# Optimization experiments

Hardware: AMD Instinct MI355X
Metric: run time of the kernel (lower is better)

Reference implementation:

```python
import jax, jax.numpy as jnp
import numpy as np

RADIUS = 0.5
NSAMPLE = 32
RATIO = 0.25
HEADS = 8


def _ln(x, g, b, eps=1e-5):
    m = x.mean(-1, keepdims=True)
    v = ((x - m) ** 2).mean(-1, keepdims=True)
    return (x - m) / jnp.sqrt(v + eps) * g + b


def _fps(xyz, M):
    """Farthest point sampling (start at index 0, matches pytorch3d default). Non-differentiable."""
    xyz = jax.lax.stop_gradient(xyz)  # mirrors @torch.no_grad
    B, N, _ = xyz.shape

    def step(carry, _):
        mind, last = carry  # (B,N), (B,)
        lastp = jnp.take_along_axis(xyz, last[:, None, None], axis=1)  # (B,1,3)
        d = jnp.sum((xyz - lastp) ** 2, axis=-1)  # (B,N)
        mind = jnp.minimum(mind, d)
        nxt = jnp.argmax(mind, axis=1).astype(jnp.int32)
        return (mind, nxt), last

    init = (jnp.full((B, N), jnp.inf, xyz.dtype), jnp.zeros((B,), jnp.int32))
    _, idx = jax.lax.scan(step, init, None, length=M)
    return idx.T  # (B,M)


def setup_inputs() -> dict:
    key = jax.random.key(0)
    ks = jax.random.split(key, 12)
    B, N, Cin, C = 2, 8192, 64, 128
    w = lambda i, shape: jax.random.normal(ks[i], shape, jnp.float32) * 0.02
    return {
        "xyz": jax.random.normal(ks[0], (B, N, 3), jnp.float32),
        "feats": jax.random.normal(ks[1], (B, N, Cin), jnp.float32),
        "W_in": w(2, (Cin, C)), "b_in": jnp.zeros((C,), jnp.float32),
        "ln_in_g": jnp.ones((C,), jnp.float32), "ln_in_b": jnp.zeros((C,), jnp.float32),
        "W_pos": w(3, (3, C)), "b_pos": jnp.zeros((C,), jnp.float32),
        "Wq": w(4, (C, C)), "bq": jnp.zeros((C,), jnp.float32),
        "Wk": w(5, (C, C)), "bk": jnp.zeros((C,), jnp.float32),
        "Wv": w(6, (C, C)), "bv": jnp.zeros((C,), jnp.float32),
        "Wo": w(7, (C, C)), "bo": jnp.zeros((C,), jnp.float32),
        "ln1_g": jnp.ones((C,), jnp.float32), "ln1_b": jnp.zeros((C,), jnp.float32),
        "W1": w(8, (C, 4 * C)), "b1": jnp.zeros((4 * C,), jnp.float32),
        "W2": w(9, (4 * C, C)), "b2": jnp.zeros((C,), jnp.float32),
        "ln2_g": jnp.ones((C,), jnp.float32), "ln2_b": jnp.zeros((C,), jnp.float32),
        "out_g": jnp.ones((C,), jnp.float32), "out_b": jnp.zeros((C,), jnp.float32),
    }


def reference(xyz, feats, W_in, b_in, ln_in_g, ln_in_b, W_pos, b_pos,
              Wq, bq, Wk, bk, Wv, bv, Wo, bo, ln1_g, ln1_b,
              W1, b1, W2, b2, ln2_g, ln2_b, out_g, out_b):
    B, N, _ = xyz.shape
    M = max(1, int(round(N * RATIO)))
    K = NSAMPLE

    # --- FPS centroids ---
    ctr_idx = _fps(xyz, M)  # (B,M) int32
    ctr_xyz = xyz[jnp.arange(B)[:, None], ctr_idx]  # (B,M,3)

    # --- ball query: first K points (by index) within radius; -1 where missing ---
    d2 = jnp.sum((ctr_xyz[:, :, None, :] - xyz[:, None, :, :]) ** 2, axis=-1)  # (B,M,N)
    within = d2 < RADIUS * RADIUS
    cand = jnp.where(within, jnp.arange(N, dtype=jnp.int32)[None, None, :], N)
    first_k = jnp.sort(cand, axis=-1)[..., :K]  # (B,M,K)
    raw_idx = jnp.where(first_k < N, first_k, -1)
    neigh_idx = jnp.where(raw_idx < 0, ctr_idx[:, :, None], raw_idx)  # fill pads with centroid

    b3 = jnp.arange(B)[:, None, None]
    neigh_xyz = xyz[b3, neigh_idx]     # (B,M,K,3)
    neigh_feats = feats[b3, neigh_idx]  # (B,M,K,Cin)

    # --- in_proj: Linear -> LayerNorm -> ReLU ---
    h = jax.nn.relu(_ln(neigh_feats @ W_in + b_in, ln_in_g, ln_in_b))  # (B,M,K,C)
    C = h.shape[-1]
    BM = B * M
    pad = (raw_idx < 0).reshape(BM, K)  # key padding mask

    # --- local transformer layer (coords -> positional embedding, post-norm) ---
    x = h.reshape(BM, K, C) + (neigh_xyz.reshape(BM, K, 3) @ W_pos + b_pos)
    H = HEADS
    Dh = C // H
    split = lambda t: t.reshape(BM, K, H, Dh).transpose(0, 2, 1, 3)  # (BM,H,K,Dh)
    q, k, v = split(x @ Wq + bq), split(x @ Wk + bk), split(x @ Wv + bv)
    scores = jnp.einsum('bhqd,bhkd->bhqk', q, k) / np.sqrt(Dh)
    scores = jnp.where(pad[:, None, None, :], -1e9, scores)
    attn = jax.nn.softmax(scores, axis=-1)
    o = jnp.einsum('bhqk,bhkd->bhqd', attn, v).transpose(0, 2, 1, 3).reshape(BM, K, C)
    x = _ln(x + o @ Wo + bo, ln1_g, ln1_b)
    x = _ln(x + jax.nn.relu(x @ W1 + b1) @ W2 + b2, ln2_g, ln2_b)

    # --- max-pool over neighbourhood, out LayerNorm ---
    pooled = _ln(x.max(axis=1).reshape(B, M, C), out_g, out_b)
    return ctr_xyz, pooled
```

## Files before the change

### kernel.cpp

```cpp
#include <hip/hip_runtime.h>
#include <math.h>

#define N_PTS 8192
#define BATCH 2
#define M_CTR 2048
#define KNB   32
#define CIN   64
#define CH    128
#define NHEAD 8
#define DH    16

typedef __attribute__((ext_vector_type(4))) float f32x4;
typedef __attribute__((ext_vector_type(8))) short bf16x8;

template<int CTRL>
__device__ __forceinline__ unsigned long long dpp_max_u64(unsigned long long k) {
  int lo = (int)(unsigned)k;
  int hi = (int)(k >> 32);
  int lo2 = __builtin_amdgcn_update_dpp(0, lo, CTRL, 0xF, 0xF, true);
  int hi2 = __builtin_amdgcn_update_dpp(0, hi, CTRL, 0xF, 0xF, true);
  unsigned long long o = ((unsigned long long)(unsigned)hi2 << 32) | (unsigned)lo2;
  return o > k ? o : k;
}

__device__ __forceinline__ unsigned long long swz16_max_u64(unsigned long long k) {
  int lo = (int)(unsigned)k;
  int hi = (int)(k >> 32);
  int lo2 = __builtin_amdgcn_ds_swizzle(lo, 0x401F);
  int hi2 = __builtin_amdgcn_ds_swizzle(hi, 0x401F);
  unsigned long long o = ((unsigned long long)(unsigned)hi2 << 32) | (unsigned)lo2;
  return o > k ? o : k;
}

__device__ __forceinline__ unsigned long long maxu64(unsigned long long a,
                                                     unsigned long long b) {
  return a > b ? a : b;
}

__global__ __launch_bounds__(512, 1) void fps_kernel(const float* __restrict__ xyz,
                                                     int* __restrict__ ctrIdx,
                                                     float* __restrict__ outCtr) {
  __shared__ float4 sxyz[N_PTS];
  __shared__ int    cidx[M_CTR];
  __shared__ __align__(16) unsigned long long candK[2][8];

  const int b = blockIdx.x;
  const int t = threadIdx.x;
  const int lane = t & 63;
  const int w = t >> 6;
  const float* xb = xyz + (size_t)b * N_PTS * 3;

  float px[16], py[16], pz[16], mind[16];
#pragma unroll
  for (int s = 0; s < 16; ++s) {
    int pt = t + s * 512;
    float x = xb[pt * 3 + 0];
    float y = xb[pt * 3 + 1];
    float z = xb[pt * 3 + 2];
    px[s] = x; py[s] = y; pz[s] = z;
    mind[s] = INFINITY;
    sxyz[pt] = make_float4(x, y, z, 0.f);
  }
  unsigned lo16[16];
#pragma unroll
  for (int s = 0; s < 16; ++s) lo16[s] = ~(unsigned)(t + s * 512);
  __syncthreads();

  int last = 0;
  for (int m = 0; m < M_CTR; ++m) {
    if (t == 0) cidx[m] = last;
    float4 lp = sxyz[last];
#pragma unroll
    for (int s = 0; s < 16; ++s) {
      float dx = __fsub_rn(px[s], lp.x);
      float dy = __fsub_rn(py[s], lp.y);
      float dz = __fsub_rn(pz[s], lp.z);
      float d2 = __fadd_rn(__fadd_rn(__fmul_rn(dx, dx), __fmul_rn(dy, dy)),
                           __fmul_rn(dz, dz));
      mind[s] = fminf(mind[s], d2);
    }
    unsigned long long key[16];
#pragma unroll
    for (int s = 0; s < 16; ++s)
      key[s] = ((unsigned long long)__float_as_uint(mind[s]) << 32) | lo16[s];
#pragma unroll
    for (int i = 0; i < 8; ++i) key[i] = maxu64(key[i], key[i + 8]);
#pragma unroll
    for (int i = 0; i < 4; ++i) key[i] = maxu64(key[i], key[i + 4]);
    key[0] = maxu64(key[0], key[2]);
    key[1] = maxu64(key[1], key[3]);
    unsigned long long k0 = maxu64(key[0], key[1]);
    k0 = dpp_max_u64<0xB1>(k0);
    k0 = dpp_max_u64<0x4E>(k0);
    k0 = dpp_max_u64<0x141>(k0);
    k0 = dpp_max_u64<0x140>(k0);
    k0 = swz16_max_u64(k0);
    k0 = maxu64(k0, (unsigned long long)__shfl_xor((unsigned long long)k0, 32, 64));
    const int buf = m & 1;
    if (lane == 0) candK[buf][w] = k0;
    __syncthreads();
    const ulonglong2* ck = (const ulonglong2*)&candK[buf][0];
    ulonglong2 c0v = ck[0], c1v = ck[1], c2v = ck[2], c3v = ck[3];
    unsigned long long m0 = maxu64(c0v.x, c0v.y);
    unsigned long long m1 = maxu64(c1v.x, c1v.y);
    unsigned long long m2 = maxu64(c2v.x, c2v.y);
    unsigned long long m3 = maxu64(c3v.x, c3v.y);
    unsigned long long best = maxu64(maxu64(m0, m1), maxu64(m2, m3));
    last = (int)(~(unsigned)best);
  }
  __syncthreads();
  for (int m = t; m < M_CTR; m += 512) {
    int ci = cidx[m];
    ctrIdx[b * M_CTR + m] = ci;
    float4 c = sxyz[ci];
    float* o = outCtr + (size_t)(b * M_CTR + m) * 3;
    o[0] = c.x; o[1] = c.y; o[2] = c.z;
  }
}

__global__ __launch_bounds__(256) void ballq_kernel(const float* __restrict__ xyz,
                                                    const int* __restrict__ ctrIdx,
                                                    int* __restrict__ rawIdx) {
  const int cm   = blockIdx.x * 4 + (threadIdx.x >> 6);
  const int lane = threadIdx.x & 63;
  const int b    = cm >> 11;
  const float* xb = xyz + (size_t)b * N_PTS * 3;
  const int ci = ctrIdx[cm];
  const float cx = xb[ci * 3 + 0], cy = xb[ci * 3 + 1], cz = xb[ci * 3 + 2];
  int* out = rawIdx + (size_t)cm * KNB;
  int have = 0;
  for (int base = 0; base < N_PTS; base += 64) {
    int pt = base + lane;
    float dx = __fsub_rn(cx, xb[pt * 3 + 0]);
    float dy = __fsub_rn(cy, xb[pt * 3 + 1]);
    float dz = __fsub_rn(cz, xb[pt * 3 + 2]);
    float d2 = __fadd_rn(__fadd_rn(__fmul_rn(dx, dx), __fmul_rn(dy, dy)),
                         __fmul_rn(dz, dz));
    bool hit = d2 < 0.25f;
    unsigned long long mask = __ballot(hit);
    if (hit) {
      int rank = have + __popcll(mask & ((1ull << lane) - 1ull));
      if (rank < KNB) out[rank] = pt;
    }
    have += __popcll(mask);
    if (have >= KNB) break;
  }
  if (lane < KNB && lane >= have) out[lane] = -1;
}

__device__ __forceinline__ unsigned short f2bf(float f) {
  unsigned u = __float_as_uint(f);
  unsigned r = (u + 0x7FFFu + ((u >> 16) & 1u)) >> 16;
  return (unsigned short)r;
}
__device__ __forceinline__ float bf2f(unsigned short s) {
  return __uint_as_float(((unsigned)s) << 16);
}

__global__ __launch_bounds__(256) void prep_kernel(const float* __restrict__ W_in,
    const float* __restrict__ Wq, const float* __restrict__ Wk,
    const float* __restrict__ Wv, const float* __restrict__ Wo,
    const float* __restrict__ W1, const float* __restrict__ W2,
    short* __restrict__ wsW) {
  int i = blockIdx.x * 256 + threadIdx.x;
  if (i >= 204800) return;
  const float* src; int K, C, off;
  if (i < 8192)        { src = W_in; K = 64;  C = 128; off = i; }
  else if (i < 24576)  { src = Wq;   K = 128; C = 128; off = i - 8192; }
  else if (i < 40960)  { src = Wk;   K = 128; C = 128; off = i - 24576; }
  else if (i < 57344)  { src = Wv;   K = 128; C = 128; off = i - 40960; }
  else if (i < 73728)  { src = Wo;   K = 128; C = 128; off = i - 57344; }
  else if (i < 139264) { src = W1;   K = 128; C = 512; off = i - 73728; }
  else                 { src = W2;   K = 512; C = 128; off = i - 139264; }
  int c = off / K, k = off - c * K;
  wsW[i] = (short)f2bf(src[(size_t)k * C + c]);
}

#define XS  136
#define VTS 40
#define PS  264

struct SAParams {
  const float* xyz; const float* feats;
  const float* b_in; const float* ln_in_g; const float* ln_in_b;
  const float* W_pos; const float* b_pos;
  const float* bq; const float* bk; const float* bv; const float* bo;
  const float* ln1_g; const float* ln1_b;
  const float* b1; const float* b2;
  const float* ln2_g; const float* ln2_b; const float* out_g; const float* out_b;
  const short* wsW;
  const int* ctrIdx; const int* rawIdx;
  float* out;
};

template<int C>
__device__ __forceinline__ float dppf(float v) {
  return __int_as_float(__builtin_amdgcn_update_dpp(0, __float_as_int(v), C, 0xF, 0xF, true));
}
__device__ __forceinline__ float red16_add(float v) {
  v += dppf<0xB1>(v);  v += dppf<0x4E>(v);
  v += dppf<0x141>(v); v += dppf<0x140>(v);
  return v;
}
__device__ __forceinline__ float red16_max(float v) {
  v = fmaxf(v, dppf<0xB1>(v));  v = fmaxf(v, dppf<0x4E>(v));
  v = fmaxf(v, dppf<0x141>(v)); v = fmaxf(v, dppf<0x140>(v));
  return v;
}

template<int NCT, int NKS>
__device__ __forceinline__ void mm_mfma(const short* __restrict__ albase, int lstr,
                                        const short* __restrict__ wt, int wK,
                                        f32x4 (&acc)[NCT], int l15, int lg) {
#pragma unroll
  for (int ks = 0; ks < NKS; ++ks) {
    bf16x8 a = *(const bf16x8*)(albase + l15 * lstr + ks * 32 + lg * 8);
#pragma unroll
    for (int ct = 0; ct < NCT; ++ct) {
      bf16x8 bf = *(const bf16x8*)(wt + (size_t)(ct * 16 + l15) * wK + ks * 32 + lg * 8);
      acc[ct] = __builtin_amdgcn_mfma_f32_16x16x32_bf16(a, bf, acc[ct], 0, 0, 0);
    }
  }
}

__global__ __launch_bounds__(128, 1) void sa_kernel(SAParams p) {
  __shared__ short sm[3 * 32 * XS + 128 * VTS + 32 * PS];
  __shared__ float nxs[32], nys[32], nzs[32];
  __shared__ int   nidx[32];
  __shared__ unsigned padmaskS;
  __shared__ float psum[2][2];

  short* const xb  = sm;
  short* const qb  = sm + 32 * XS;
  short* const kb  = sm + 2 * 32 * XS;
  short* const vT  = sm + 3 * 32 * XS;
  short* const Pb  = sm + 3 * 32 * XS + 128 * VTS;
  short* const fsb = Pb;
  short* const ob  = qb;
  short* const hb  = kb;

  const int t    = threadIdx.x;
  const int lane = t & 63;
  const int rt   = t >> 6;
  const int l15  = lane & 15;
  const int lg   = lane >> 4;
  const int cm   = blockIdx.x;
  const int b    = cm >> 11;
  const short* arow = 0;

  if (t < 32) {
    int raw = p.rawIdx[(size_t)cm * KNB + t];
    int ci  = p.ctrIdx[cm];
    int ni  = (raw < 0) ? ci : raw;
    nidx[t] = ni;
    const float* q = p.xyz + ((size_t)b * N_PTS + ni) * 3;
    nxs[t] = q[0]; nys[t] = q[1]; nzs[t] = q[2];
  }
  if (t < 64) {
    bool isPad = (t < 32) ? (p.rawIdx[(size_t)cm * KNB + t] < 0) : false;
    unsigned long long m = __ballot(isPad);
    if (t == 0) padmaskS = (unsigned)m;
  }
  __syncthreads();

  {
    int row = t >> 2;
    int cs  = (t & 3) * 16;
    const float* src = p.feats + ((size_t)b * N_PTS + nidx[row]) * CIN + cs;
    float4 f0 = *(const float4*)(src + 0);
    float4 f1 = *(const float4*)(src + 4);
    float4 f2 = *(const float4*)(src + 8);
    float4 f3 = *(const float4*)(src + 12);
    unsigned short u[16];
#pragma unroll
    for (int j = 0; j < 4; ++j) {
      u[j]      = f2bf((&f0.x)[j]); u[4 + j]  = f2bf((&f1.x)[j]);
      u[8 + j]  = f2bf((&f2.x)[j]); u[12 + j] = f2bf((&f3.x)[j]);
    }
    uint4 w0, w1;
    unsigned* uw = (unsigned*)&w0;
#pragma unroll
    for (int j = 0; j < 8; ++j) ((unsigned*)&w0)[j < 4 ? j : j] = 0;
    (void)uw;
    unsigned packed[8];
#pragma unroll
    for (int j = 0; j < 8; ++j) packed[j] = (unsigned)u[2 * j] | ((unsigned)u[2 * j + 1] << 16);
    w0 = make_uint4(packed[0], packed[1], packed[2], packed[3]);
    w1 = make_uint4(packed[4], packed[5], packed[6], packed[7]);
    *(uint4*)(fsb + row * 72 + cs)     = w0;
    *(uint4*)(fsb + row * 72 + cs + 8) = w1;
  }
  __syncthreads();

  const unsigned padmask = padmaskS;
  float rowxyz[3][4];
#pragma unroll
  for (int r = 0; r < 4; ++r) {
    int row = rt * 16 + lg * 4 + r;
    rowxyz[0][r] = nxs[row]; rowxyz[1][r] = nys[row]; rowxyz[2][r] = nzs[row];
  }

  {
    f32x4 acc[8] = {};
    mm_mfma<8, 2>(fsb + rt * 16 * 72, 72, p.wsW + 0, 64, acc, l15, lg);
    float s[4] = {}, sq[4] = {};
#pragma unroll
    for (int ct = 0; ct < 8; ++ct) {
      float bia = p.b_in[ct * 16 + l15];
#pragma unroll
      for (int r = 0; r < 4; ++r) {
        acc[ct][r] += bia;
        s[r] += acc[ct][r]; sq[r] += acc[ct][r] * acc[ct][r];
      }
    }
    float mean[4], inv[4];
#pragma unroll
    for (int r = 0; r < 4; ++r) {
      float S = red16_add(s[r]), SQ = red16_add(sq[r]);
      mean[r] = S * (1.0f / CH);
      float var = fmaxf(SQ * (1.0f / CH) - mean[r] * mean[r], 0.f);
      inv[r] = rsqrtf(var + 1e-5f);
    }
#pragma unroll
    for (int ct = 0; ct < 8; ++ct) {
      int c = ct * 16 + l15;
      float g  = p.ln_in_g[c], bt = p.ln_in_b[c];
      float w0 = p.W_pos[0 * CH + c], w1 = p.W_pos[1 * CH + c];
      float w2 = p.W_pos[2 * CH + c], bp = p.b_pos[c];
#pragma unroll
      for (int r = 0; r < 4; ++r) {
        int row = rt * 16 + lg * 4 + r;
        float h = (acc[ct][r] - mean[r]) * inv[r] * g + bt;
        h = fmaxf(h, 0.f);
        float pos = fmaf(rowxyz[0][r], w0, fmaf(rowxyz[1][r], w1,
                    fmaf(rowxyz[2][r], w2, bp)));
        xb[row * XS + c] = (short)f2bf(h + pos);
      }
    }
  }
  __syncthreads();

  arow = xb + rt * 16 * XS;
  {
    f32x4 acc[8] = {};
    mm_mfma<8, 4>(arow, XS, p.wsW + 8192, 128, acc, l15, lg);
#pragma unroll
    for (int ct = 0; ct < 8; ++ct) {
      int c = ct * 16 + l15;
      float bia = p.bq[c];
#pragma unroll
      for (int r = 0; r < 4; ++r)
        qb[(rt * 16 + lg * 4 + r) * XS + c] = (short)f2bf((acc[ct][r] + bia) * 0.25f);
    }
  }
  {
    f32x4 acc[8] = {};
    mm_mfma<8, 4>(arow, XS, p.wsW + 24576, 128, acc, l15, lg);
#pragma unroll
    for (int ct = 0; ct < 8; ++ct) {
      int c = ct * 16 + l15;
      float bia = p.bk[c];
#pragma unroll
      for (int r = 0; r < 4; ++r)
        kb[(rt * 16 + lg * 4 + r) * XS + c] = (short)f2bf(acc[ct][r] + bia);
    }
  }
  {
    f32x4 acc[8] = {};
    mm_mfma<8, 4>(arow, XS, p.wsW + 40960, 128, acc, l15, lg);
#pragma unroll
    for (int ct = 0; ct < 8; ++ct) {
      int c = ct * 16 + l15;
      float bia = p.bv[c];
#pragma unroll
      for (int r = 0; r < 4; ++r)
        vT[c * VTS + rt * 16 + lg * 4 + r] = (short)f2bf(acc[ct][r] + bia);
    }
  }
  __syncthreads();

  {
    bool pad0 = (padmask >> l15) & 1u;
    bool pad1 = (padmask >> (16 + l15)) & 1u;
    const bf16x8 z = {0, 0, 0, 0, 0, 0, 0, 0};
#pragma unroll
    for (int h = 0; h < NHEAD; ++h) {
      bf16x8 a = *(const bf16x8*)(qb + (rt * 16 + l15) * XS + h * DH + (lg & 1) * 8);
      if (lg >= 2) a = z;
      bf16x8 b0 = *(const bf16x8*)(kb + (l15) * XS + h * DH + (lg & 1) * 8);
      bf16x8 b1 = *(const bf16x8*)(kb + (16 + l15) * XS + h * DH + (lg & 1) * 8);
      f32x4 s0 = {}, s1 = {};
      s0 = __builtin_amdgcn_mfma_f32_16x16x32_bf16(a, b0, s0, 0, 0, 0);
      s1 = __builtin_amdgcn_mfma_f32_16x16x32_bf16(a, b1, s1, 0, 0, 0);
#pragma unroll
      for (int r = 0; r < 4; ++r) {
        float v0 = pad0 ? -1e9f : s0[r];
        float v1 = pad1 ? -1e9f : s1[r];
        float mx = red16_max(fmaxf(v0, v1));
        float e0 = __expf(v0 - mx), e1 = __expf(v1 - mx);
        float sum = red16_add(e0 + e1);
        float isum = 1.0f / sum;
        int row = rt * 16 + lg * 4 + r;
        Pb[row * PS + h * 32 + l15]      = (short)f2bf(e0 * isum);
        Pb[row * PS + h * 32 + 16 + l15] = (short)f2bf(e1 * isum);
      }
    }
  }
  __syncthreads();

  {
#pragma unroll
    for (int h = 0; h < NHEAD; ++h) {
      bf16x8 a  = *(const bf16x8*)(Pb + (rt * 16 + l15) * PS + h * 32 + lg * 8);
      bf16x8 bf = *(const bf16x8*)(vT + (h * DH + l15) * VTS + lg * 8);
      f32x4 o = {};
      o = __builtin_amdgcn_mfma_f32_16x16x32_bf16(a, bf, o, 0, 0, 0);
#pragma unroll
      for (int r = 0; r < 4; ++r)
        ob[(rt * 16 + lg * 4 + r) * XS + h * DH + l15] = (short)f2bf(o[r]);
    }
  }

  {
    f32x4 acc[8] = {};
    mm_mfma<8, 4>(ob + rt * 16 * XS, XS, p.wsW + 57344, 128, acc, l15, lg);
    float s[4] = {}, sq[4] = {};
#pragma unroll
    for (int ct = 0; ct < 8; ++ct) {
      int c = ct * 16 + l15;
      float bia = p.bo[c];
#pragma unroll
      for (int r = 0; r < 4; ++r) {
        int row = rt * 16 + lg * 4 + r;
        acc[ct][r] += bia + bf2f((unsigned short)xb[row * XS + c]);
        s[r] += acc[ct][r]; sq[r] += acc[ct][r] * acc[ct][r];
      }
    }
    float mean[4], inv[4];
#pragma unroll
    for (int r = 0; r < 4; ++r) {
      float S = red16_add(s[r]), SQ = red16_add(sq[r]);
      mean[r] = S * (1.0f / CH);
      float var = fmaxf(SQ * (1.0f / CH) - mean[r] * mean[r], 0.f);
      inv[r] = rsqrtf(var + 1e-5f);
    }
#pragma unroll
    for (int ct = 0; ct < 8; ++ct) {
      int c = ct * 16 + l15;
      float g = p.ln1_g[c], bt = p.ln1_b[c];
#pragma unroll
      for (int r = 0; r < 4; ++r) {
        int row = rt * 16 + lg * 4 + r;
        xb[row * XS + c] = (short)f2bf((acc[ct][r] - mean[r]) * inv[r] * g + bt);
      }
    }
  }

  {
    f32x4 acc2[8] = {};
#pragma unroll
    for (int cb = 0; cb < 4; ++cb) {
      f32x4 acch[8] = {};
      mm_mfma<8, 4>(xb + rt * 16 * XS, XS, p.wsW + 73728 + cb * 128 * 128, 128,
                    acch, l15, lg);
#pragma unroll
      for (int ct = 0; ct < 8; ++ct) {
        int c = ct * 16 + l15;
        float bia = p.b1[cb * 128 + c];
#pragma unroll
        for (int r = 0; r < 4; ++r)
          hb[(rt * 16 + lg * 4 + r) * XS + c] = (short)f2bf(fmaxf(acch[ct][r] + bia, 0.f));
      }
      __syncthreads();
      mm_mfma<8, 4>(hb + rt * 16 * XS, XS, p.wsW + 139264 + cb * 128, 512,
                    acc2, l15, lg);
      __syncthreads();
    }
    float s[4] = {}, sq[4] = {};
#pragma unroll
    for (int ct = 0; ct < 8; ++ct) {
      int c = ct * 16 + l15;
      float bia = p.b2[c];
#pragma unroll
      for (int r = 0; r < 4; ++r) {
        int row = rt * 16 + lg * 4 + r;
        acc2[ct][r] += bia + bf2f((unsigned short)xb[row * XS + c]);
        s[r] += acc2[ct][r]; sq[r] += acc2[ct][r] * acc2[ct][r];
      }
    }
    float mean[4], inv[4];
#pragma unroll
    for (int r = 0; r < 4; ++r) {
      float S = red16_add(s[r]), SQ = red16_add(sq[r]);
      mean[r] = S * (1.0f / CH);
      float var = fmaxf(SQ * (1.0f / CH) - mean[r] * mean[r], 0.f);
      inv[r] = rsqrtf(var + 1e-5f);
    }
#pragma unroll
    for (int ct = 0; ct < 8; ++ct) {
      int c = ct * 16 + l15;
      float g = p.ln2_g[c], bt = p.ln2_b[c];
#pragma unroll
      for (int r = 0; r < 4; ++r) {
        int row = rt * 16 + lg * 4 + r;
        xb[row * XS + c] = (short)f2bf((acc2[ct][r] - mean[r]) * inv[r] * g + bt);
      }
    }
  }
  __syncthreads();

  {
    float mx = -INFINITY;
#pragma unroll 8
    for (int r = 0; r < KNB; ++r) mx = fmaxf(mx, bf2f((unsigned short)xb[r * XS + t]));
    float s = mx, sq = mx * mx;
#pragma unroll
    for (int off = 1; off < 64; off <<= 1) {
      s  += __shfl_xor(s,  off, 64);
      sq += __shfl_xor(sq, off, 64);
    }
    if (lane == 0) { psum[rt][0] = s; psum[rt][1] = sq; }
    __syncthreads();
    float S = psum[0][0] + psum[1][0];
    float SQ = psum[0][1] + psum[1][1];
    float mean = S * (1.0f / CH);
    float var = fmaxf(SQ * (1.0f / CH) - mean * mean, 0.f);
    float inv = rsqrtf(var + 1e-5f);
    p.out[(size_t)BATCH * M_CTR * 3 + (size_t)cm * CH + t] =
        (mx - mean) * inv * p.out_g[t] + p.out_b[t];
  }
}

extern "C" void kernel_launch(void* const* d_in, const int* in_sizes, int n_in,
                              void* d_out, int out_size, void* d_ws, size_t ws_size,
                              hipStream_t stream) {
  const float* xyz     = (const float*)d_in[0];
  const float* feats   = (const float*)d_in[1];
  const float* W_in    = (const float*)d_in[2];
  const float* b_in    = (const float*)d_in[3];
  const float* ln_in_g = (const float*)d_in[4];
  const float* ln_in_b = (const float*)d_in[5];
  const float* W_pos   = (const float*)d_in[6];
  const float* b_pos   = (const float*)d_in[7];
  const float* Wq      = (const float*)d_in[8];
  const float* bq      = (const float*)d_in[9];
  const float* Wk      = (const float*)d_in[10];
  const float* bk      = (const float*)d_in[11];
  const float* Wv      = (const float*)d_in[12];
  const float* bv      = (const float*)d_in[13];
  const float* Wo      = (const float*)d_in[14];
  const float* bo      = (const float*)d_in[15];
  const float* ln1_g   = (const float*)d_in[16];
  const float* ln1_b   = (const float*)d_in[17];
  const float* W1      = (const float*)d_in[18];
  const float* b1      = (const float*)d_in[19];
  const float* W2      = (const float*)d_in[20];
  const float* b2      = (const float*)d_in[21];
  const float* ln2_g   = (const float*)d_in[22];
  const float* ln2_b   = (const float*)d_in[23];
  const float* out_g   = (const float*)d_in[24];
  const float* out_b   = (const float*)d_in[25];
  float* out = (float*)d_out;

  int* wsCtr = (int*)d_ws;
  int* wsRaw = wsCtr + BATCH * M_CTR;
  short* wsW = (short*)(wsRaw + BATCH * M_CTR * KNB);

  prep_kernel<<<(204800 + 255) / 256, 256, 0, stream>>>(W_in, Wq, Wk, Wv, Wo,
                                                        W1, W2, wsW);
  fps_kernel<<<BATCH, 512, 0, stream>>>(xyz, wsCtr, out);
  ballq_kernel<<<(BATCH * M_CTR) / 4, 256, 0, stream>>>(xyz, wsCtr, wsRaw);

  SAParams p{xyz, feats, b_in, ln_in_g, ln_in_b, W_pos, b_pos,
             bq, bk, bv, bo, ln1_g, ln1_b, b1, b2,
             ln2_g, ln2_b, out_g, out_b,
             wsW, wsCtr, wsRaw, out};
  sa_kernel<<<BATCH * M_CTR, 128, 0, stream>>>(p);
}
```

Measured before the change: 2.348 ms.

## Widen FPS to 1024 threads with LDS atomicMax reduction and inline center writes

```diff
diff --git a/kernel.cpp b/kernel.cpp
--- a/kernel.cpp
+++ b/kernel.cpp
@@ -37,84 +37,67 @@
   return a > b ? a : b;
 }
 
-__global__ __launch_bounds__(512, 1) void fps_kernel(const float* __restrict__ xyz,
-                                                     int* __restrict__ ctrIdx,
-                                                     float* __restrict__ outCtr) {
+__global__ __launch_bounds__(1024, 1) void fps_kernel(const float* __restrict__ xyz,
+                                                      int* __restrict__ ctrIdx,
+                                                      float* __restrict__ outCtr) {
   __shared__ float4 sxyz[N_PTS];
-  __shared__ int    cidx[M_CTR];
-  __shared__ __align__(16) unsigned long long candK[2][8];
+  __shared__ unsigned long long redK[4];
 
   const int b = blockIdx.x;
   const int t = threadIdx.x;
   const int lane = t & 63;
-  const int w = t >> 6;
   const float* xb = xyz + (size_t)b * N_PTS * 3;
 
-  float px[16], py[16], pz[16], mind[16];
-#pragma unroll
-  for (int s = 0; s < 16; ++s) {
-    int pt = t + s * 512;
+  float px[8], py[8], pz[8], mind[8];
+  unsigned lo8[8];
+#pragma unroll
+  for (int s = 0; s < 8; ++s) {
+    int pt = t + s * 1024;
     float x = xb[pt * 3 + 0];
     float y = xb[pt * 3 + 1];
     float z = xb[pt * 3 + 2];
     px[s] = x; py[s] = y; pz[s] = z;
     mind[s] = INFINITY;
+    lo8[s] = ~(unsigned)pt;
     sxyz[pt] = make_float4(x, y, z, 0.f);
   }
-  unsigned lo16[16];
-#pragma unroll
-  for (int s = 0; s < 16; ++s) lo16[s] = ~(unsigned)(t + s * 512);
+  if (t < 3) redK[t] = 0ull;
   __syncthreads();
 
   int last = 0;
   for (int m = 0; m < M_CTR; ++m) {
-    if (t == 0) cidx[m] = last;
     float4 lp = sxyz[last];
-#pragma unroll
-    for (int s = 0; s < 16; ++s) {
+    if (t == 0) {
+      ctrIdx[b * M_CTR + m] = last;
+      float* o = outCtr + (size_t)(b * M_CTR + m) * 3;
+      o[0] = lp.x; o[1] = lp.y; o[2] = lp.z;
+    }
+    unsigned long long c0 = 0ull, c1 = 0ull;
+#pragma unroll
+    for (int s = 0; s < 8; ++s) {
       float dx = __fsub_rn(px[s], lp.x);
       float dy = __fsub_rn(py[s], lp.y);
       float dz = __fsub_rn(pz[s], lp.z);
       float d2 = __fadd_rn(__fadd_rn(__fmul_rn(dx, dx), __fmul_rn(dy, dy)),
                            __fmul_rn(dz, dz));
-      mind[s] = fminf(mind[s], d2);
-    }
-    unsigned long long key[16];
-#pragma unroll
-    for (int s = 0; s < 16; ++s)
-      key[s] = ((unsigned long long)__float_as_uint(mind[s]) << 32) | lo16[s];
-#pragma unroll
-    for (int i = 0; i < 8; ++i) key[i] = maxu64(key[i], key[i + 8]);
-#pragma unroll
-    for (int i = 0; i < 4; ++i) key[i] = maxu64(key[i], key[i + 4]);
-    key[0] = maxu64(key[0], key[2]);
-    key[1] = maxu64(key[1], key[3]);
-    unsigned long long k0 = maxu64(key[0], key[1]);
+      float mn = fminf(mind[s], d2);
+      mind[s] = mn;
+      unsigned long long key =
+          ((unsigned long long)__float_as_uint(mn) << 32) | lo8[s];
+      if (s & 1) c1 = maxu64(c1, key); else c0 = maxu64(c0, key);
+    }
+    unsigned long long k0 = maxu64(c0, c1);
     k0 = dpp_max_u64<0xB1>(k0);
     k0 = dpp_max_u64<0x4E>(k0);
     k0 = dpp_max_u64<0x141>(k0);
     k0 = dpp_max_u64<0x140>(k0);
     k0 = swz16_max_u64(k0);
-    k0 = maxu64(k0, (unsigned long long)__shfl_xor((unsigned long long)k0, 32, 64));
-    const int buf = m & 1;
-    if (lane == 0) candK[buf][w] = k0;
+    const int buf = m % 3;
+    if ((lane & 31) == 0)
+      atomicMax((unsigned long long*)&redK[buf], k0);
+    if (t == 1) redK[(m + 1) % 3] = 0ull;
     __syncthreads();
-    const ulonglong2* ck = (const ulonglong2*)&candK[buf][0];
-    ulonglong2 c0v = ck[0], c1v = ck[1], c2v = ck[2], c3v = ck[3];
-    unsigned long long m0 = maxu64(c0v.x, c0v.y);
-    unsigned long long m1 = maxu64(c1v.x, c1v.y);
-    unsigned long long m2 = maxu64(c2v.x, c2v.y);
-    unsigned long long m3 = maxu64(c3v.x, c3v.y);
-    unsigned long long best = maxu64(maxu64(m0, m1), maxu64(m2, m3));
-    last = (int)(~(unsigned)best);
-  }
-  __syncthreads();
-  for (int m = t; m < M_CTR; m += 512) {
-    int ci = cidx[m];
-    ctrIdx[b * M_CTR + m] = ci;
-    float4 c = sxyz[ci];
-    float* o = outCtr + (size_t)(b * M_CTR + m) * 3;
-    o[0] = c.x; o[1] = c.y; o[2] = c.z;
+    last = (int)(~(unsigned)redK[buf]);
   }
 }
 
@@ -277,16 +260,11 @@
       u[j]      = f2bf((&f0.x)[j]); u[4 + j]  = f2bf((&f1.x)[j]);
       u[8 + j]  = f2bf((&f2.x)[j]); u[12 + j] = f2bf((&f3.x)[j]);
     }
-    uint4 w0, w1;
-    unsigned* uw = (unsigned*)&w0;
-#pragma unroll
-    for (int j = 0; j < 8; ++j) ((unsigned*)&w0)[j < 4 ? j : j] = 0;
-    (void)uw;
     unsigned packed[8];
 #pragma unroll
     for (int j = 0; j < 8; ++j) packed[j] = (unsigned)u[2 * j] | ((unsigned)u[2 * j + 1] << 16);
-    w0 = make_uint4(packed[0], packed[1], packed[2], packed[3]);
-    w1 = make_uint4(packed[4], packed[5], packed[6], packed[7]);
+    uint4 w0 = make_uint4(packed[0], packed[1], packed[2], packed[3]);
+    uint4 w1 = make_uint4(packed[4], packed[5], packed[6], packed[7]);
     *(uint4*)(fsb + row * 72 + cs)     = w0;
     *(uint4*)(fsb + row * 72 + cs + 8) = w1;
   }
@@ -568,7 +546,7 @@
 
   prep_kernel<<<(204800 + 255) / 256, 256, 0, stream>>>(W_in, Wq, Wk, Wv, Wo,
                                                         W1, W2, wsW);
-  fps_kernel<<<BATCH, 512, 0, stream>>>(xyz, wsCtr, out);
+  fps_kernel<<<BATCH, 1024, 0, stream>>>(xyz, wsCtr, out);
   ballq_kernel<<<(BATCH * M_CTR) / 4, 256, 0, stream>>>(xyz, wsCtr, wsRaw);
 
   SAParams p{xyz, feats, b_in, ln_in_g, ln_in_b, W_pos, b_pos,
```

Result: slower. 2.638 ms (+12.3%).
